# Optimization experiments

Measured on AMD Instinct MI355X. Metric: run time of the kernel, lower is better.

Reference implementation:

```python
import jax, jax.numpy as jnp
import numpy as np

N = 1024                      # FFT length (init kwarg)
NF = N // 2 + 1               # rfft output length = len(freq)
PB_LO = 40.0 / 60.0           # pulse_band[0] in Hz
PB_HI = 180.0 / 60.0          # pulse_band[1] in Hz
DELTA_HZ = 6.0 / 60.0         # self.delta after /60
W0, W1 = 1.0, 1.0             # weights[0], weights[1]
B, T = 32768, 1024


def setup_inputs() -> dict:
    key = jax.random.key(0)
    k1, k2 = jax.random.split(key)
    preds = jax.random.normal(k1, (B, T), dtype=jnp.float32)
    # realistic camera frame rates ~25-35 Hz (must exceed 2*pulse_band[1]=6 Hz)
    Fs = 25.0 + 10.0 * jax.random.uniform(k2, (B,), dtype=jnp.float32)
    return {"preds": preds, "Fs": Fs}


def reference(preds, Fs):
    idx = jnp.arange(NF)                                            # [Nf]
    # freq = linspace(0, Fs/2, Nf) per sample -> [B, Nf]
    freq = (Fs[:, None] * 0.5) * (idx.astype(jnp.float32) / (NF - 1))
    left = jnp.argmin(jnp.abs(freq - PB_LO), axis=1)                # [B] int
    right = jnp.argmin(jnp.abs(freq - PB_HI), axis=1)               # [B] int

    psd = jnp.abs(jnp.fft.rfft(preds, n=N)) ** 2                    # [B, Nf]
    total = jnp.sum(psd, axis=-1)                                   # [B]

    l = left[:, None]
    r = right[:, None]
    out_band = (idx < l) | (idx >= r)                               # psd[:left] + psd[right:]
    band_loss = jnp.sum(jnp.where(out_band, psd, 0.0), axis=-1) / (1e-8 + total)

    in_band = (idx >= l) & (idx < r)
    # argmax(psd[left:right]) + left  (psd >= 0, so -inf mask is safe)
    peak = jnp.argmax(jnp.where(in_band, psd, -jnp.inf), axis=1)    # [B]
    # delta = max(1, round(self.delta / (Fs/2/len(freq))))  (round half-to-even, as Python)
    delta = jnp.maximum(1.0, jnp.round(DELTA_HZ / (Fs * 0.5 / NF))).astype(jnp.int32)

    p = peak[:, None]
    d = delta[:, None]
    # psd[left:peak-delta] + psd[peak+delta:right]  (empty slices -> 0 via mask)
    sparse_mask = in_band & ((idx < p - d) | (idx >= p + d))
    num = jnp.sum(jnp.where(sparse_mask, psd, 0.0), axis=-1)
    # sum(psd[left:right] + 1e-8) adds 1e-8 per in-band bin, keep faithful
    den = jnp.sum(jnp.where(in_band, psd + 1e-8, 0.0), axis=-1)
    sparse_loss = num / den

    return W0 * jnp.mean(band_loss) + W1 * jnp.mean(sparse_loss)
```

## Files before the change

kernel.cpp:

```cpp
#include <hip/hip_runtime.h>
#include <cmath>

#define BATCH 32768

struct cplx { float x, y; };
__device__ __forceinline__ cplx cadd(cplx a, cplx b){ return {a.x+b.x, a.y+b.y}; }
__device__ __forceinline__ cplx csub(cplx a, cplx b){ return {a.x-b.x, a.y-b.y}; }
__device__ __forceinline__ cplx cmul(cplx a, cplx b){ return {a.x*b.x - a.y*b.y, a.x*b.y + a.y*b.x}; }
__device__ __forceinline__ cplx cmul_mi(cplx a){ return {a.y, -a.x}; }
__device__ __forceinline__ cplx cmul_w81(cplx a){ const float c=0.70710678f; return {c*(a.x+a.y), c*(a.y-a.x)}; }
__device__ __forceinline__ cplx cmul_w83(cplx a){ const float c=0.70710678f; return {c*(a.y-a.x), -c*(a.x+a.y)}; }

__device__ __forceinline__ void dft8(cplx a[8]) {
    cplx t0=cadd(a[0],a[4]), t4=csub(a[0],a[4]);
    cplx t1=cadd(a[1],a[5]), t5=csub(a[1],a[5]);
    cplx t2=cadd(a[2],a[6]), t6=csub(a[2],a[6]);
    cplx t3=cadd(a[3],a[7]), t7=csub(a[3],a[7]);
    cplx u0=cadd(t0,t2), u2=csub(t0,t2);
    cplx u1=cadd(t1,t3), u3=cmul_mi(csub(t1,t3));
    a[0]=cadd(u0,u1); a[4]=csub(u0,u1); a[2]=cadd(u2,u3); a[6]=csub(u2,u3);
    cplx v0=t4, v1=cmul_w81(t5), v2=cmul_mi(t6), v3=cmul_w83(t7);
    cplx w0=cadd(v0,v2), w2=csub(v0,v2);
    cplx w1=cadd(v1,v3), w3=cmul_mi(csub(v1,v3));
    a[1]=cadd(w0,w1); a[5]=csub(w0,w1); a[3]=cadd(w2,w3); a[7]=csub(w2,w3);
}

__device__ __forceinline__ int nearest_bin(float fs, float target) {
    float x = target * 1024.0f / fs;
    int i0 = (int)floorf(x);
    int lo = max(0, i0 - 1), hi = min(512, i0 + 2);
    int bi = lo; float bd = 1e30f;
    for (int i = lo; i <= hi; ++i) {
        float fr = (fs * 0.5f) * ((float)i / 512.0f);
        float d = fabsf(fr - target);
        if (d < bd) { bd = d; bi = i; }
    }
    return bi;
}

__global__ __launch_bounds__(256) void fft_loss_kernel(
    const float* __restrict__ preds, const float* __restrict__ Fs,
    float* __restrict__ blockpartial)
{
    __shared__ float sre[4][576];
    __shared__ float sim[4][576];
    __shared__ float sblk[4];

    const int tid  = threadIdx.x;
    const int wv   = tid >> 6;
    const int lane = tid & 63;
    const int row  = blockIdx.x * 4 + wv;

    float* re = sre[wv];
    float* im = sim[wv];

    const float2* x2 = reinterpret_cast<const float2*>(preds) + (size_t)row * 512;

    cplx z[8];
#pragma unroll
    for (int n1 = 0; n1 < 8; ++n1) {
        float2 v = x2[n1 * 64 + lane];
        z[n1] = {v.x, v.y};
    }
    dft8(z);
    {
        float sb, cb;
        __sincosf(-0.012271846f * (float)lane, &sb, &cb);
        cplx w = {cb, sb}, u = w;
#pragma unroll
        for (int r = 1; r < 8; ++r) { z[r] = cmul(z[r], u); u = cmul(u, w); }
    }
#pragma unroll
    for (int r = 0; r < 8; ++r) { re[r*72 + lane] = z[r].x; im[r*72 + lane] = z[r].y; }

    const int rB = lane & 7, m0 = lane >> 3;
    cplx b[8];
#pragma unroll
    for (int m1 = 0; m1 < 8; ++m1) {
        int a = rB*72 + 8*m1 + m0;
        b[m1] = {re[a], im[a]};
    }
    dft8(b);
    {
        float sb, cb;
        __sincosf(-0.09817477f * (float)m0, &sb, &cb);
        cplx w = {cb, sb}, u = w;
#pragma unroll
        for (int s = 1; s < 8; ++s) { b[s] = cmul(b[s], u); u = cmul(u, w); }
    }
#pragma unroll
    for (int s = 0; s < 8; ++s) {
        int a = rB*72 + 8*m0 + ((s + m0) & 7);
        re[a] = b[s].x; im[a] = b[s].y;
    }

    const int sC = lane >> 3;
    cplx c[8];
#pragma unroll
    for (int m = 0; m < 8; ++m) {
        int a = rB*72 + 8*m + ((sC + m) & 7);
        c[m] = {re[a], im[a]};
    }
    dft8(c);
#pragma unroll
    for (int t = 0; t < 8; ++t) { re[lane + 64*t] = c[t].x; im[lane + 64*t] = c[t].y; }

    const float fs  = Fs[row];
    const int left  = nearest_bin(fs, (float)(40.0/60.0));
    const int right = nearest_bin(fs, 3.0f);

    float psd[8];
    float total = 0.f, inb = 0.f, best = -1.f;
    int besti = 1 << 30;
    float sk, ck;
    __sincosf(-0.0061359233f * (float)lane, &sk, &ck);
    cplx wk = {ck, sk};
    const cplx wstep = {0.92387953f, -0.38268343f};
#pragma unroll
    for (int t = 0; t < 8; ++t) {
        int k  = lane + 64*t;
        cplx a  = {re[k], im[k]};
        int k2 = (512 - k) & 511;
        cplx bb = {re[k2], -im[k2]};
        float ex = 0.5f*(a.x + bb.x), ey = 0.5f*(a.y + bb.y);
        float dx = a.x - bb.x,        dy = a.y - bb.y;
        float ox = 0.5f*dy,           oy = -0.5f*dx;
        float Xr = ex + wk.x*ox - wk.y*oy;
        float Xi = ey + wk.x*oy + wk.y*ox;
        float v  = Xr*Xr + Xi*Xi;
        psd[t] = v;
        total += v;
        if (k >= left && k < right) {
            inb += v;
            if (v > best) { best = v; besti = k; }
        }
        wk = cmul(wk, wstep);
    }
    float psd512 = 0.f;
    if (lane == 0) {
        float d = re[0] - im[0];
        psd512 = d*d;
        total += psd512;
    }
#pragma unroll
    for (int t = 0; t < 8; ++t) im[lane + 64*t] = psd[t];
    if (lane == 0) im[512] = psd512;

#pragma unroll
    for (int off = 32; off > 0; off >>= 1) {
        total += __shfl_down(total, off);
        inb   += __shfl_down(inb, off);
        float ob = __shfl_down(best, off);
        int   oi = __shfl_down(besti, off);
        if (ob > best || (ob == best && oi < besti)) { best = ob; besti = oi; }
    }
    if (lane == 0) {
        int delta = (int)rintf(0.1f / ((fs * 0.5f) / 513.0f));
        if (delta < 1) delta = 1;
        int lo = max(left, besti - delta), hi = min(right, besti + delta);
        float wsum = 0.f;
        for (int f = lo; f < hi; ++f) wsum += im[f];
        float band = (total - inb) / (1e-8f + total);
        float den  = inb + 1e-8f * (float)(right - left);
        sblk[wv] = band + (inb - wsum) / den;
    }
    __syncthreads();
    if (tid == 0) blockpartial[blockIdx.x] = sblk[0] + sblk[1] + sblk[2] + sblk[3];
}

__global__ __launch_bounds__(1024) void reduce_kernel(
    const float* __restrict__ bp, float* __restrict__ out)
{
    __shared__ float w[16];
    const int t = threadIdx.x;
    float acc = 0.f;
#pragma unroll
    for (int i = 0; i < 8; ++i) acc += bp[t + 1024*i];
    for (int off = 32; off > 0; off >>= 1) acc += __shfl_down(acc, off);
    const int lane = t & 63, wvi = t >> 6;
    if (lane == 0) w[wvi] = acc;
    __syncthreads();
    if (t == 0) {
        float s = 0.f;
        for (int i = 0; i < 16; ++i) s += w[i];
        out[0] = s * (1.0f / (float)BATCH);
    }
}

extern "C" void kernel_launch(void* const* d_in, const int* in_sizes, int n_in,
                              void* d_out, int out_size, void* d_ws, size_t ws_size,
                              hipStream_t stream) {
    const float* preds = (const float*)d_in[0];
    const float* Fs    = (const float*)d_in[1];
    float* bp          = (float*)d_ws;
    float* out         = (float*)d_out;

    fft_loss_kernel<<<BATCH / 4, 256, 0, stream>>>(preds, Fs, bp);
    reduce_kernel<<<1, 1024, 0, stream>>>(bp, out);
}
```

Measured before the change: 192.0 us.

## Fuse final reduction via last-block atomic counter and use shuffles for conjugate bins

Removes the separate reduce kernel: each block stores its partial sum and bumps an atomic counter, and the last block reduces all partials. A memset of the counter is added to the launch instead. The final-stage results now stay in registers, and the conjugate-symmetric bin is fetched with a wave shuffle instead of a shared-memory round trip. Twiddle factors are computed directly rather than by a serial recurrence, and the Fs load is hoisted to the kernel start. The ideas are mixed, and the memset still adds a small launch.

```diff
diff --git a/kernel.cpp b/kernel.cpp
--- a/kernel.cpp
+++ b/kernel.cpp
@@ -40,11 +40,12 @@
 
 __global__ __launch_bounds__(256) void fft_loss_kernel(
     const float* __restrict__ preds, const float* __restrict__ Fs,
-    float* __restrict__ blockpartial)
+    float* __restrict__ bp, unsigned* __restrict__ cnt, float* __restrict__ out)
 {
     __shared__ float sre[4][576];
     __shared__ float sim[4][576];
     __shared__ float sblk[4];
+    __shared__ int lastFlag;
 
     const int tid  = threadIdx.x;
     const int wv   = tid >> 6;
@@ -54,6 +55,8 @@
     float* re = sre[wv];
     float* im = sim[wv];
 
+    const float fs = Fs[row];
+
     const float2* x2 = reinterpret_cast<const float2*>(preds) + (size_t)row * 512;
 
     cplx z[8];
@@ -66,9 +69,15 @@
     {
         float sb, cb;
         __sincosf(-0.012271846f * (float)lane, &sb, &cb);
-        cplx w = {cb, sb}, u = w;
-#pragma unroll
-        for (int r = 1; r < 8; ++r) { z[r] = cmul(z[r], u); u = cmul(u, w); }
+        cplx w1 = {cb, sb};
+        cplx w2 = cmul(w1, w1);
+        cplx w3 = cmul(w2, w1);
+        cplx w4 = cmul(w2, w2);
+        cplx w5 = cmul(w4, w1);
+        cplx w6 = cmul(w4, w2);
+        cplx w7 = cmul(w4, w3);
+        z[1]=cmul(z[1],w1); z[2]=cmul(z[2],w2); z[3]=cmul(z[3],w3); z[4]=cmul(z[4],w4);
+        z[5]=cmul(z[5],w5); z[6]=cmul(z[6],w6); z[7]=cmul(z[7],w7);
     }
 #pragma unroll
     for (int r = 0; r < 8; ++r) { re[r*72 + lane] = z[r].x; im[r*72 + lane] = z[r].y; }
@@ -84,9 +93,15 @@
     {
         float sb, cb;
         __sincosf(-0.09817477f * (float)m0, &sb, &cb);
-        cplx w = {cb, sb}, u = w;
-#pragma unroll
-        for (int s = 1; s < 8; ++s) { b[s] = cmul(b[s], u); u = cmul(u, w); }
+        cplx w1 = {cb, sb};
+        cplx w2 = cmul(w1, w1);
+        cplx w3 = cmul(w2, w1);
+        cplx w4 = cmul(w2, w2);
+        cplx w5 = cmul(w4, w1);
+        cplx w6 = cmul(w4, w2);
+        cplx w7 = cmul(w4, w3);
+        b[1]=cmul(b[1],w1); b[2]=cmul(b[2],w2); b[3]=cmul(b[3],w3); b[4]=cmul(b[4],w4);
+        b[5]=cmul(b[5],w5); b[6]=cmul(b[6],w6); b[7]=cmul(b[7],w7);
     }
 #pragma unroll
     for (int s = 0; s < 8; ++s) {
@@ -102,49 +117,49 @@
         c[m] = {re[a], im[a]};
     }
     dft8(c);
-#pragma unroll
-    for (int t = 0; t < 8; ++t) { re[lane + 64*t] = c[t].x; im[lane + 64*t] = c[t].y; }
-
-    const float fs  = Fs[row];
+
     const int left  = nearest_bin(fs, (float)(40.0/60.0));
     const int right = nearest_bin(fs, 3.0f);
 
-    float psd[8];
     float total = 0.f, inb = 0.f, best = -1.f;
     int besti = 1 << 30;
     float sk, ck;
     __sincosf(-0.0061359233f * (float)lane, &sk, &ck);
-    cplx wk = {ck, sk};
-    const cplx wstep = {0.92387953f, -0.38268343f};
+    const cplx wb = {ck, sk};
+    const float c16r[8] = { 1.f,  0.92387953f,  0.70710678f,  0.38268343f,
+                            0.f, -0.38268343f, -0.70710678f, -0.92387953f };
+    const float c16i[8] = { 0.f, -0.38268343f, -0.70710678f, -0.92387953f,
+                           -1.f, -0.92387953f, -0.70710678f, -0.38268343f };
+    const int srcl = (64 - lane) & 63;
+    const bool l0 = (lane == 0);
 #pragma unroll
     for (int t = 0; t < 8; ++t) {
         int k  = lane + 64*t;
-        cplx a  = {re[k], im[k]};
-        int k2 = (512 - k) & 511;
-        cplx bb = {re[k2], -im[k2]};
-        float ex = 0.5f*(a.x + bb.x), ey = 0.5f*(a.y + bb.y);
-        float dx = a.x - bb.x,        dy = a.y - bb.y;
-        float ox = 0.5f*dy,           oy = -0.5f*dx;
+        cplx a = c[t];
+        float pxr = __shfl(c[7-t].x, srcl);
+        float pxi = __shfl(c[7-t].y, srcl);
+        float bx = l0 ? c[(8-t)&7].x : pxr;
+        float by = l0 ? c[(8-t)&7].y : pxi;
+        float ex = 0.5f*(a.x + bx), ey = 0.5f*(a.y - by);
+        float dx = a.x - bx,        dy = a.y + by;
+        float ox = 0.5f*dy,          oy = -0.5f*dx;
+        cplx wk = cmul(wb, {c16r[t], c16i[t]});
         float Xr = ex + wk.x*ox - wk.y*oy;
         float Xi = ey + wk.x*oy + wk.y*ox;
         float v  = Xr*Xr + Xi*Xi;
-        psd[t] = v;
+        re[k] = v;
         total += v;
         if (k >= left && k < right) {
             inb += v;
             if (v > best) { best = v; besti = k; }
         }
-        wk = cmul(wk, wstep);
-    }
-    float psd512 = 0.f;
+    }
     if (lane == 0) {
-        float d = re[0] - im[0];
-        psd512 = d*d;
-        total += psd512;
-    }
-#pragma unroll
-    for (int t = 0; t < 8; ++t) im[lane + 64*t] = psd[t];
-    if (lane == 0) im[512] = psd512;
+        float d = c[0].x - c[0].y;
+        float p512 = d*d;
+        total += p512;
+        re[512] = p512;
+    }
 
 #pragma unroll
     for (int off = 32; off > 0; off >>= 1) {
@@ -159,31 +174,34 @@
         if (delta < 1) delta = 1;
         int lo = max(left, besti - delta), hi = min(right, besti + delta);
         float wsum = 0.f;
-        for (int f = lo; f < hi; ++f) wsum += im[f];
+        for (int f = lo; f < hi; ++f) wsum += re[f];
         float band = (total - inb) / (1e-8f + total);
         float den  = inb + 1e-8f * (float)(right - left);
         sblk[wv] = band + (inb - wsum) / den;
     }
     __syncthreads();
-    if (tid == 0) blockpartial[blockIdx.x] = sblk[0] + sblk[1] + sblk[2] + sblk[3];
-}
-
-__global__ __launch_bounds__(1024) void reduce_kernel(
-    const float* __restrict__ bp, float* __restrict__ out)
-{
-    __shared__ float w[16];
-    const int t = threadIdx.x;
-    float acc = 0.f;
-#pragma unroll
-    for (int i = 0; i < 8; ++i) acc += bp[t + 1024*i];
-    for (int off = 32; off > 0; off >>= 1) acc += __shfl_down(acc, off);
-    const int lane = t & 63, wvi = t >> 6;
-    if (lane == 0) w[wvi] = acc;
+
+    if (tid == 0) {
+        float blocksum = sblk[0] + sblk[1] + sblk[2] + sblk[3];
+        __hip_atomic_store(&bp[blockIdx.x], blocksum, __ATOMIC_RELEASE,
+                           __HIP_MEMORY_SCOPE_AGENT);
+        unsigned old = __hip_atomic_fetch_add(cnt, 1u, __ATOMIC_ACQ_REL,
+                                              __HIP_MEMORY_SCOPE_AGENT);
+        lastFlag = (old == (unsigned)(gridDim.x - 1));
+    }
     __syncthreads();
-    if (t == 0) {
-        float s = 0.f;
-        for (int i = 0; i < 16; ++i) s += w[i];
-        out[0] = s * (1.0f / (float)BATCH);
+    if (lastFlag) {
+        float acc = 0.f;
+#pragma unroll
+        for (int j = 0; j < 32; ++j)
+            acc += __hip_atomic_load(&bp[tid + 256*j], __ATOMIC_RELAXED,
+                                     __HIP_MEMORY_SCOPE_AGENT);
+#pragma unroll
+        for (int off = 32; off > 0; off >>= 1) acc += __shfl_down(acc, off);
+        if (lane == 0) sblk[wv] = acc;
+        __syncthreads();
+        if (tid == 0)
+            out[0] = (sblk[0] + sblk[1] + sblk[2] + sblk[3]) * (1.0f / (float)BATCH);
     }
 }
 
@@ -193,8 +211,7 @@
     const float* preds = (const float*)d_in[0];
     const float* Fs    = (const float*)d_in[1];
     float* bp          = (float*)d_ws;
-    float* out         = (float*)d_out;
-
-    fft_loss_kernel<<<BATCH / 4, 256, 0, stream>>>(preds, Fs, bp);
-    reduce_kernel<<<1, 1024, 0, stream>>>(bp, out);
-}
+    unsigned* cnt      = (unsigned*)((char*)d_ws + 32768);
+    hipMemsetAsync(cnt, 0, sizeof(unsigned), stream);
+    fft_loss_kernel<<<BATCH / 4, 256, 0, stream>>>(preds, Fs, bp, cnt, (float*)d_out);
+}
```

Measured after the change: 646.3 us. +236.6%, slower.
